# Performance work log

Measured on AMD Instinct MI355X. Metric: run time of the kernel, lower is better.

## Reference

```python
import jax, jax.numpy as jnp
import numpy as np

L, V, P, D, H, F = 6, 50257, 1024, 1024, 16, 4096
DH = D // H
EPS = 1e-5


def setup_inputs() -> dict:
    key = jax.random.key(0)
    ks = jax.random.split(key, 8)
    s = 0.02  # init scale to keep activations sane across layers
    inp = {
        "input_ids": jax.random.randint(ks[0], (2, 1024), 0, V),
        "wte": jax.random.normal(ks[1], (V, D), jnp.float32) * s,
        "wpe": jax.random.normal(ks[2], (P, D), jnp.float32) * s,
        "ln1_g": jnp.ones((L, D), jnp.float32),
        "ln1_b": jnp.zeros((L, D), jnp.float32),
        "wq": jax.random.normal(ks[3], (L, D, D), jnp.float32) * s,
        "bq": jnp.zeros((L, D), jnp.float32),
        "wk": jax.random.normal(ks[4], (L, D, D), jnp.float32) * s,
        "bk": jnp.zeros((L, D), jnp.float32),
        "wv": jax.random.normal(ks[5], (L, D, D), jnp.float32) * s,
        "bv": jnp.zeros((L, D), jnp.float32),
        "wo": jax.random.normal(jax.random.fold_in(key, 10), (L, D, D), jnp.float32) * s,
        "bo": jnp.zeros((L, D), jnp.float32),
        "ln2_g": jnp.ones((L, D), jnp.float32),
        "ln2_b": jnp.zeros((L, D), jnp.float32),
        "w1": jax.random.normal(ks[6], (L, D, F), jnp.float32) * s,
        "b1": jnp.zeros((L, F), jnp.float32),
        "w2": jax.random.normal(ks[7], (L, F, D), jnp.float32) * s,
        "b2": jnp.zeros((L, D), jnp.float32),
        "lnf_g": jnp.ones((D,), jnp.float32),
        "lnf_b": jnp.zeros((D,), jnp.float32),
    }
    return inp


def _ln(x, g, b):
    m = jnp.mean(x, axis=-1, keepdims=True)
    v = jnp.mean(jnp.square(x - m), axis=-1, keepdims=True)
    return (x - m) * jax.lax.rsqrt(v + EPS) * g + b


def _block(x, p):
    (g1, be1, wq, bq, wk, bk, wv, bv, wo, bo, g2, be2, w1, b1, w2, b2) = p
    B, T, _ = x.shape
    h = _ln(x, g1, be1)
    q = (h @ wq + bq).reshape(B, T, H, DH)
    k = (h @ wk + bk).reshape(B, T, H, DH)
    v = (h @ wv + bv).reshape(B, T, H, DH)
    scores = jnp.einsum("bqhd,bkhd->bhqk", q, k) * (1.0 / np.sqrt(DH))
    attn = jax.nn.softmax(scores, axis=-1)  # NOTE: no causal mask (as in source)
    o = jnp.einsum("bhqk,bkhd->bqhd", attn, v).reshape(B, T, D)
    x = x + o @ wo + bo
    h2 = _ln(x, g2, be2)
    x = x + jax.nn.gelu(h2 @ w1 + b1, approximate=False) @ w2 + b2
    return x


def reference(input_ids, wte, wpe, ln1_g, ln1_b, wq, bq, wk, bk, wv, bv,
              wo, bo, ln2_g, ln2_b, w1, b1, w2, b2, lnf_g, lnf_b):
    T = input_ids.shape[1]
    x = wte[input_ids] + wpe[:T]  # [B,T,D]
    params = (ln1_g, ln1_b, wq, bq, wk, bk, wv, bv, wo, bo,
              ln2_g, ln2_b, w1, b1, w2, b2)

    def step(x, p):
        return _block(x, p), None

    x, _ = jax.lax.scan(step, x, params)
    return _ln(x, lnf_g, lnf_b)
```

## Files before the change

### kernel.cpp

```cpp
#include <hip/hip_runtime.h>
#include <hip/hip_bf16.h>
#include <math.h>

#define DV 1024
#define FF 4096
#define NLAY 6
#define NH 16
#define TT 1024
#define NTOK 2048

typedef float f32x4 __attribute__((ext_vector_type(4)));
typedef short bf16x8 __attribute__((ext_vector_type(8)));
typedef unsigned short u16;
typedef u16 u16x4 __attribute__((ext_vector_type(4)));
typedef u16 u16x8 __attribute__((ext_vector_type(8)));

__device__ __forceinline__ u16 f2b(float f) {
  unsigned u = __float_as_uint(f);
  unsigned r = (u + 0x7fffu + ((u >> 16) & 1u)) >> 16;
  return (u16)r;
}
__device__ __forceinline__ float b2f(u16 u) {
  return __uint_as_float(((unsigned)u) << 16);
}

__device__ __forceinline__ void gload_lds16(const void* g, void* lds) {
  __builtin_amdgcn_global_load_lds(
      (const __attribute__((address_space(1))) void*)g,
      (__attribute__((address_space(3))) void*)lds, 16, 0, 0);
}

__global__ __launch_bounds__(256) void embed_ln_k(const int* __restrict__ ids,
                                                  const float* __restrict__ wte,
                                                  const float* __restrict__ wpe,
                                                  const float* __restrict__ gg,
                                                  const float* __restrict__ bb,
                                                  float* __restrict__ X,
                                                  u16* __restrict__ outb) {
  int row = blockIdx.x, tid = threadIdx.x;
  int t = row & (TT - 1);
  int id = ids[row];
  f32x4 a = *(const f32x4*)(wte + (size_t)id * DV + tid * 4);
  f32x4 p = *(const f32x4*)(wpe + (size_t)t * DV + tid * 4);
  f32x4 v = a + p;
  *(f32x4*)(X + (size_t)row * DV + tid * 4) = v;
  float s1 = v[0] + v[1] + v[2] + v[3];
  float s2 = v[0] * v[0] + v[1] * v[1] + v[2] * v[2] + v[3] * v[3];
#pragma unroll
  for (int o = 32; o >= 1; o >>= 1) {
    s1 += __shfl_xor(s1, o);
    s2 += __shfl_xor(s2, o);
  }
  __shared__ float sh[8];
  int w = tid >> 6;
  if ((tid & 63) == 0) { sh[w] = s1; sh[w + 4] = s2; }
  __syncthreads();
  s1 = sh[0] + sh[1] + sh[2] + sh[3];
  s2 = sh[4] + sh[5] + sh[6] + sh[7];
  float mean = s1 * (1.0f / DV);
  float var = s2 * (1.0f / DV) - mean * mean;
  float rstd = rsqrtf(var + 1e-5f);
  f32x4 gv = *(const f32x4*)(gg + tid * 4);
  f32x4 bv = *(const f32x4*)(bb + tid * 4);
  u16x4 r;
#pragma unroll
  for (int i = 0; i < 4; ++i) r[i] = f2b((v[i] - mean) * rstd * gv[i] + bv[i]);
  *(u16x4*)(outb + (size_t)row * DV + tid * 4) = r;
}

template <int OUTF>
__global__ __launch_bounds__(256) void ln_k(const float* __restrict__ X,
                                            const float* __restrict__ gg,
                                            const float* __restrict__ bb,
                                            u16* __restrict__ outb,
                                            float* __restrict__ outf) {
  int row = blockIdx.x, tid = threadIdx.x;
  f32x4 v = *(const f32x4*)(X + (size_t)row * DV + tid * 4);
  float s1 = v[0] + v[1] + v[2] + v[3];
  float s2 = v[0] * v[0] + v[1] * v[1] + v[2] * v[2] + v[3] * v[3];
#pragma unroll
  for (int o = 32; o >= 1; o >>= 1) {
    s1 += __shfl_xor(s1, o);
    s2 += __shfl_xor(s2, o);
  }
  __shared__ float sh[8];
  int w = tid >> 6;
  if ((tid & 63) == 0) { sh[w] = s1; sh[w + 4] = s2; }
  __syncthreads();
  s1 = sh[0] + sh[1] + sh[2] + sh[3];
  s2 = sh[4] + sh[5] + sh[6] + sh[7];
  float mean = s1 * (1.0f / DV);
  float var = s2 * (1.0f / DV) - mean * mean;
  float rstd = rsqrtf(var + 1e-5f);
  f32x4 gv = *(const f32x4*)(gg + tid * 4);
  f32x4 bv = *(const f32x4*)(bb + tid * 4);
  f32x4 o;
#pragma unroll
  for (int i = 0; i < 4; ++i) o[i] = (v[i] - mean) * rstd * gv[i] + bv[i];
  if (OUTF) {
    *(f32x4*)(outf + (size_t)row * DV + tid * 4) = o;
  } else {
    u16x4 r = {f2b(o[0]), f2b(o[1]), f2b(o[2]), f2b(o[3])};
    *(u16x4*)(outb + (size_t)row * DV + tid * 4) = r;
  }
}

template <int NS, int OUTF>
__global__ __launch_bounds__(256) void reduce_ln_k(
    float* __restrict__ X, const u16* __restrict__ pp,
    const float* __restrict__ bias, const float* __restrict__ gg,
    const float* __restrict__ bb, u16* __restrict__ outb,
    float* __restrict__ outf) {
  int row = blockIdx.x, tid = threadIdx.x;
  size_t off = (size_t)row * DV + tid * 4;
  f32x4 v = *(const f32x4*)(X + off);
  if (NS > 0) {
    f32x4 bvv = *(const f32x4*)(bias + tid * 4);
    v += bvv;
#pragma unroll
    for (int s = 0; s < NS; ++s) {
      u16x4 pv = *(const u16x4*)(pp + (size_t)s * NTOK * DV + off);
      v[0] += b2f(pv[0]); v[1] += b2f(pv[1]);
      v[2] += b2f(pv[2]); v[3] += b2f(pv[3]);
    }
    *(f32x4*)(X + off) = v;
  }
  float s1 = v[0] + v[1] + v[2] + v[3];
  float s2 = v[0] * v[0] + v[1] * v[1] + v[2] * v[2] + v[3] * v[3];
#pragma unroll
  for (int o = 32; o >= 1; o >>= 1) {
    s1 += __shfl_xor(s1, o);
    s2 += __shfl_xor(s2, o);
  }
  __shared__ float sh[8];
  int w = tid >> 6;
  if ((tid & 63) == 0) { sh[w] = s1; sh[w + 4] = s2; }
  __syncthreads();
  s1 = sh[0] + sh[1] + sh[2] + sh[3];
  s2 = sh[4] + sh[5] + sh[6] + sh[7];
  float mean = s1 * (1.0f / DV);
  float var = s2 * (1.0f / DV) - mean * mean;
  float rstd = rsqrtf(var + 1e-5f);
  f32x4 gv = *(const f32x4*)(gg + tid * 4);
  f32x4 bv = *(const f32x4*)(bb + tid * 4);
  f32x4 o;
#pragma unroll
  for (int i = 0; i < 4; ++i) o[i] = (v[i] - mean) * rstd * gv[i] + bv[i];
  if (OUTF) {
    *(f32x4*)(outf + off) = o;
  } else {
    u16x4 r = {f2b(o[0]), f2b(o[1]), f2b(o[2]), f2b(o[3])};
    *(u16x4*)(outb + off) = r;
  }
}

__global__ __launch_bounds__(256) void transw_k(const float* __restrict__ wq,
                                                const float* __restrict__ wk,
                                                const float* __restrict__ wv,
                                                const float* __restrict__ wo,
                                                const float* __restrict__ w1,
                                                const float* __restrict__ w2,
                                                u16* __restrict__ WT) {
  int lay = blockIdx.y;
  size_t oDD = (size_t)lay * DV * DV, oDF = (size_t)lay * DV * FF;
  u16* WTL = WT + (size_t)lay * 12 * 1024 * 1024;
  int bid = blockIdx.x;
  const float* src;
  u16* dst;
  int K, N, tile;
  if (bid < 256) {
    int which = bid >> 6;
    src = (which == 0 ? wq : which == 1 ? wk : which == 2 ? wv : wo) + oDD;
    dst = WTL + (size_t)which * (DV * DV);
    K = DV; N = DV; tile = bid & 63;
  } else if (bid < 512) {
    src = w1 + oDF; dst = WTL + (size_t)4 * (DV * DV); K = DV; N = FF; tile = bid - 256;
  } else {
    src = w2 + oDF; dst = WTL + (size_t)8 * (DV * DV); K = FF; N = DV; tile = bid - 512;
  }
  int ntc = N >> 8;
  int tr = tile / ntc, tc = tile - tr * ntc;
  int k0 = tr * 64, n0 = tc * 256;
  __shared__ u16 ts[64][258];
  int tid = threadIdx.x, l = tid & 63, w = tid >> 6;
  f32x4 vv[16];
#pragma unroll
  for (int i = 0; i < 16; ++i)
    vv[i] = *(const f32x4*)(src + (size_t)(k0 + i * 4 + w) * N + n0 + l * 4);
#pragma unroll
  for (int i = 0; i < 16; ++i) {
    u16x4 c = {f2b(vv[i][0]), f2b(vv[i][1]), f2b(vv[i][2]), f2b(vv[i][3])};
    *(u16x4*)(&ts[i * 4 + w][l * 4]) = c;
  }
  __syncthreads();
  int kk = (tid & 7) * 8, nn = tid >> 3;
#pragma unroll
  for (int j = 0; j < 8; ++j) {
    int n = j * 32 + nn;
    u16x8 ov;
#pragma unroll
    for (int m = 0; m < 8; ++m) ov[m] = ts[kk + m][n];
    *(u16x8*)(dst + (size_t)(n0 + n) * K + k0 + kk) = ov;
  }
}

template <int EPI>
__global__ __launch_bounds__(512) void gemm_k(
    const u16* __restrict__ A, const u16* __restrict__ Wt,
    const float* __restrict__ b0, const float* __restrict__ b1,
    const float* __restrict__ b2v, u16* __restrict__ o0, u16* __restrict__ o1,
    u16* __restrict__ o2t, u16* __restrict__ op, float* __restrict__ of,
    const float* __restrict__ res, int M, int N, int K, int KS) {
  int z = blockIdx.z;
  const u16* W = Wt;
  const float* bias = b0;
  u16* outb = o0;
  if (EPI == 0) {
    W = Wt + (size_t)z * N * K;
    bias = z == 0 ? b0 : z == 1 ? b1 : b2v;
    outb = z == 0 ? o0 : o1;
  }
  int gx = gridDim.x, nwg = gx * gridDim.y;
  int lin = blockIdx.y * gx + blockIdx.x;
  int cpx = nwg >> 3;
  int swz = (lin & 7) * cpx + (lin >> 3);
  int bm = (swz % gx) * 128, bn = (swz / gx) * 128;
  int kbeg = (EPI == 3) ? z * KS : 0;
  int klen = (EPI == 3) ? KS : K;
  __shared__ __attribute__((aligned(16))) u16 SM[32768];
  u16* As = SM;
  u16* Bs = SM + 16384;
  u16* Cs = SM;
  int tid = threadIdx.x, l = tid & 63, w = tid >> 6;
  int q = l & 15, g = l >> 4;
  int wm = (w >> 1) * 32, wn = (w & 1) * 64;
  int srow = w * 16 + (l >> 3);
  int scol = (((l & 7) ^ ((l >> 3) & 7))) * 8;
  const u16* Ab = A + (size_t)(bm + srow) * K + kbeg + scol;
  const u16* Wb = W + (size_t)(bn + srow) * K + kbeg + scol;
  f32x4 acc[2][4] = {};
  int nk = klen >> 6;
#pragma unroll
  for (int i = 0; i < 2; ++i) {
    gload_lds16(Ab + (size_t)i * 8 * K, &As[(w * 16 + i * 8) * 64]);
    gload_lds16(Wb + (size_t)i * 8 * K, &Bs[(w * 16 + i * 8) * 64]);
  }
  __syncthreads();
  for (int t = 0; t < nk; ++t) {
    int cur = t & 1;
    if (t + 1 < nk) {
      int ko = (t + 1) * 64;
#pragma unroll
      for (int i = 0; i < 2; ++i) {
        gload_lds16(Ab + (size_t)i * 8 * K + ko,
                    &As[(cur ^ 1) * 8192 + (w * 16 + i * 8) * 64]);
        gload_lds16(Wb + (size_t)i * 8 * K + ko,
                    &Bs[(cur ^ 1) * 8192 + (w * 16 + i * 8) * 64]);
      }
    }
#pragma unroll
    for (int kk = 0; kk < 2; ++kk) {
      bf16x8 af[2], bfr[4];
#pragma unroll
      for (int f = 0; f < 2; ++f) {
        int ra = wm + f * 16 + q;
        af[f] = *(const bf16x8*)(&As[cur * 8192 + ra * 64 + ((kk * 4 + g) ^ (ra & 7)) * 8]);
      }
#pragma unroll
      for (int f = 0; f < 4; ++f) {
        int rb = wn + f * 16 + q;
        bfr[f] = *(const bf16x8*)(&Bs[cur * 8192 + rb * 64 + ((kk * 4 + g) ^ (rb & 7)) * 8]);
      }
#pragma unroll
      for (int fm = 0; fm < 2; ++fm)
#pragma unroll
        for (int fn = 0; fn < 4; ++fn)
          acc[fm][fn] = __builtin_amdgcn_mfma_f32_16x16x32_bf16(af[fm], bfr[fn],
                                                                acc[fm][fn], 0, 0, 0);
    }
    __syncthreads();
  }
  if (EPI == 2) {
#pragma unroll
    for (int fm = 0; fm < 2; ++fm)
#pragma unroll
      for (int fn = 0; fn < 4; ++fn) {
        int gcol = bn + wn + fn * 16 + q;
        int growb = bm + wm + fm * 16 + g * 4;
        float bv = bias[gcol];
#pragma unroll
        for (int r = 0; r < 4; ++r)
          of[(size_t)(growb + r) * N + gcol] = res[(size_t)(growb + r) * N + gcol]
                                               + acc[fm][fn][r] + bv;
      }
    return;
  }
  bool tr = (EPI == 0 && z == 2);
#pragma unroll
  for (int fm = 0; fm < 2; ++fm) {
#pragma unroll
    for (int fn = 0; fn < 4; ++fn) {
      int cL = wn + fn * 16 + q;
      float bv = (EPI == 3) ? 0.0f : bias[bn + cL];
#pragma unroll
      for (int r = 0; r < 4; ++r) {
        int rL = wm + fm * 16 + g * 4 + r;
        float v = acc[fm][fn][r] + bv;
        if (EPI == 1) v = 0.5f * v * (1.0f + erff(v * 0.70710678118f));
        if (EPI == 0 && z == 0) v *= 0.125f;
        if (tr) Cs[cL * 132 + rL] = f2b(v);
        else    Cs[rL * 132 + cL] = f2b(v);
      }
    }
  }
  __syncthreads();
  {
    int rowL = tid >> 4, c8 = (tid & 15) * 8;
#pragma unroll
    for (int p = 0; p < 4; ++p) {
      int row = p * 32 + rowL;
      u16x4 lo = *(const u16x4*)(&Cs[row * 132 + c8]);
      u16x4 hi = *(const u16x4*)(&Cs[row * 132 + c8 + 4]);
      u16x8 ov = {lo[0], lo[1], lo[2], lo[3], hi[0], hi[1], hi[2], hi[3]};
      if (tr) {
        *(u16x8*)(o2t + (size_t)(bn + row) * M + bm + c8) = ov;
      } else if (EPI == 3) {
        *(u16x8*)(op + (size_t)z * M * N + (size_t)(bm + row) * N + bn + c8) = ov;
      } else {
        *(u16x8*)(outb + (size_t)(bm + row) * N + bn + c8) = ov;
      }
    }
  }
}

__global__ __launch_bounds__(256) void attn_k(const u16* __restrict__ Q,
                                              const u16* __restrict__ Kb,
                                              const u16* __restrict__ Vt,
                                              u16* __restrict__ O) {
  int bid = blockIdx.x;
  int qt = bid & 15, h = (bid >> 4) & 15, b = bid >> 8;
  int tid = threadIdx.x, l = tid & 63, w = tid >> 6;
  int q = l & 15, g = l >> 4;
  int tokbase = b * TT;
  int qbase = tokbase + qt * 64 + w * 16;
  __shared__ __attribute__((aligned(16))) u16 Ks[2][64 * 64];
  __shared__ __attribute__((aligned(16))) u16 Vs[2][64 * 64];
  __shared__ __attribute__((aligned(16))) u16 Ps[4][1024];
  bf16x8 qf[2];
  {
    int qrow = qbase + q;
#pragma unroll
    for (int half = 0; half < 2; ++half)
      qf[half] = *(const bf16x8*)(Q + (size_t)qrow * DV + h * 64 + half * 32 + g * 8);
  }
  int rr = tid >> 3, cc = tid & 7;
  const u16* ksrc = Kb + (size_t)(tokbase + rr) * DV + h * 64 + ((cc ^ (rr & 7)) * 8);
  const u16* vsrc = Vt + (size_t)(h * 64 + rr) * NTOK + tokbase + ((cc ^ (rr & 7)) * 8);
  const size_t kst = (size_t)32 * DV;
  const size_t vst = (size_t)32 * NTOK;
  f32x4 oacc[4] = {};
  float m_run = -INFINITY, l_run = 0.0f;
#define AST(bb_, t)                                                      \
  {                                                                      \
    gload_lds16(ksrc + (size_t)(t) * 64 * DV, &Ks[bb_][tid * 8]);        \
    gload_lds16(ksrc + (size_t)(t) * 64 * DV + kst, &Ks[bb_][2048 + tid * 8]); \
    gload_lds16(vsrc + (t) * 64, &Vs[bb_][tid * 8]);                     \
    gload_lds16(vsrc + (t) * 64 + vst, &Vs[bb_][2048 + tid * 8]);        \
  }
  AST(0, 0);
  __syncthreads();
  const int nkb = TT / 64;
  for (int kbk = 0; kbk < nkb; ++kbk) {
    int cur = kbk & 1;
    if (kbk + 1 < nkb) AST(cur ^ 1, kbk + 1);
    f32x4 s[4] = {};
#pragma unroll
    for (int kt = 0; kt < 4; ++kt) {
      int row = kt * 16 + q;
#pragma unroll
      for (int half = 0; half < 2; ++half) {
        int chunk = (half * 4 + g) ^ (row & 7);
        bf16x8 kf = *(const bf16x8*)(&Ks[cur][row * 64 + chunk * 8]);
        s[kt] = __builtin_amdgcn_mfma_f32_16x16x32_bf16(kf, qf[half], s[kt], 0, 0, 0);
      }
    }
    float tmax = -INFINITY;
#pragma unroll
    for (int kt = 0; kt < 4; ++kt)
#pragma unroll
      for (int r = 0; r < 4; ++r) tmax = fmaxf(tmax, s[kt][r]);
    tmax = fmaxf(tmax, __shfl_xor(tmax, 16));
    tmax = fmaxf(tmax, __shfl_xor(tmax, 32));
    if (!__all(tmax <= m_run + 8.0f)) {
      float m_new = fmaxf(m_run, tmax);
      float corr = __expf(m_run - m_new);
      float corr4[4];
#pragma unroll
      for (int r = 0; r < 4; ++r) corr4[r] = __shfl(corr, g * 4 + r);
#pragma unroll
      for (int nt = 0; nt < 4; ++nt)
#pragma unroll
        for (int r = 0; r < 4; ++r) oacc[nt][r] *= corr4[r];
      l_run *= corr;
      m_run = m_new;
    }
    float psum = 0.0f;
    u16x4 pb[4];
#pragma unroll
    for (int kt = 0; kt < 4; ++kt)
#pragma unroll
      for (int r = 0; r < 4; ++r) {
        float p = __expf(s[kt][r] - m_run);
        psum += p;
        pb[kt][r] = f2b(p);
      }
    psum += __shfl_xor(psum, 16);
    psum += __shfl_xor(psum, 32);
    l_run += psum;
#pragma unroll
    for (int kt = 0; kt < 4; ++kt)
      *(u16x4*)(&Ps[w][q * 64 + ((kt * 4 + g) ^ (q & 7)) * 4]) = pb[kt];
#pragma unroll
    for (int kt2 = 0; kt2 < 2; ++kt2) {
      int c0 = kt2 * 8 + (g >> 1) * 4 + (g & 1) * 2;
      u16x4 a0 = *(const u16x4*)(&Ps[w][q * 64 + ((c0) ^ (q & 7)) * 4]);
      u16x4 a1 = *(const u16x4*)(&Ps[w][q * 64 + ((c0 + 1) ^ (q & 7)) * 4]);
      bf16x8 pa = {(short)a0[0], (short)a0[1], (short)a0[2], (short)a0[3],
                   (short)a1[0], (short)a1[1], (short)a1[2], (short)a1[3]};
#pragma unroll
      for (int nt = 0; nt < 4; ++nt) {
        int vrow = nt * 16 + q;
        int vc = (kt2 * 4 + g) ^ (vrow & 7);
        bf16x8 vf = *(const bf16x8*)(&Vs[cur][vrow * 64 + vc * 8]);
        oacc[nt] = __builtin_amdgcn_mfma_f32_16x16x32_bf16(pa, vf, oacc[nt], 0, 0, 0);
      }
    }
    __syncthreads();
  }
#undef AST
  float rl[4];
#pragma unroll
  for (int r = 0; r < 4; ++r) rl[r] = 1.0f / __shfl(l_run, g * 4 + r);
#pragma unroll
  for (int nt = 0; nt < 4; ++nt)
#pragma unroll
    for (int r = 0; r < 4; ++r) {
      int qrw = qbase + g * 4 + r;
      int d = nt * 16 + q;
      O[(size_t)qrw * DV + h * 64 + d] = f2b(oacc[nt][r] * rl[r]);
    }
}

extern "C" void kernel_launch(void* const* d_in, const int* in_sizes, int n_in,
                              void* d_out, int out_size, void* d_ws, size_t ws_size,
                              hipStream_t stream) {
  const int*   ids = (const int*)d_in[0];
  const float* wte = (const float*)d_in[1];
  const float* wpe = (const float*)d_in[2];
  const float* l1g = (const float*)d_in[3];
  const float* l1b = (const float*)d_in[4];
  const float* wq  = (const float*)d_in[5];
  const float* bq  = (const float*)d_in[6];
  const float* wk  = (const float*)d_in[7];
  const float* bk  = (const float*)d_in[8];
  const float* wv  = (const float*)d_in[9];
  const float* bv  = (const float*)d_in[10];
  const float* wo  = (const float*)d_in[11];
  const float* bo  = (const float*)d_in[12];
  const float* l2g = (const float*)d_in[13];
  const float* l2b = (const float*)d_in[14];
  const float* w1  = (const float*)d_in[15];
  const float* b1  = (const float*)d_in[16];
  const float* w2  = (const float*)d_in[17];
  const float* b2  = (const float*)d_in[18];
  const float* lfg = (const float*)d_in[19];
  const float* lfb = (const float*)d_in[20];
  (void)in_sizes; (void)n_in; (void)out_size;

  bool bigws = ws_size >= ((size_t)221 << 20);
  bool midws = ws_size >= ((size_t)101 << 20);

  char* ws = (char*)d_ws;
  float* x   = (float*)(ws + 0);
  u16*   hb  = (u16*)(ws + ((size_t)8 << 20));
  u16*   qb  = (u16*)(ws + ((size_t)12 << 20));
  u16*   kb  = (u16*)(ws + ((size_t)16 << 20));
  u16*   vbt = (u16*)(ws + ((size_t)20 << 20));
  u16*   ab  = (u16*)(ws + ((size_t)24 << 20));
  u16*   mb  = (u16*)(ws + ((size_t)28 << 20));
  u16*   pp  = (u16*)(ws + ((size_t)44 << 20));
  u16*   WT  = (u16*)(ws + ((size_t)(midws ? 76 : 44) << 20));

  if (bigws)
    transw_k<<<dim3(768, 6), 256, 0, stream>>>(wq, wk, wv, wo, w1, w2, WT);
  embed_ln_k<<<NTOK, 256, 0, stream>>>(ids, wte, wpe, l1g, l1b, x, hb);

  for (int lay = 0; lay < NLAY; ++lay) {
    size_t oDD = (size_t)lay * DV * DV;
    size_t oDF = (size_t)lay * DV * FF;
    u16* WTL = bigws ? WT + (size_t)lay * 12 * 1024 * 1024 : WT;
    if (!bigws)
      transw_k<<<dim3(768, 1), 256, 0, stream>>>(wq + oDD, wk + oDD, wv + oDD,
                                                 wo + oDD, w1 + oDF, w2 + oDF, WTL);
    gemm_k<0><<<dim3(16, 8, 3), 512, 0, stream>>>(
        hb, WTL, bq + lay * DV, bk + lay * DV, bv + lay * DV,
        qb, kb, vbt, nullptr, nullptr, nullptr, NTOK, DV, DV, 0);
    attn_k<<<512, 256, 0, stream>>>(qb, kb, vbt, ab);
    if (midws) {
      gemm_k<3><<<dim3(16, 8, 2), 512, 0, stream>>>(
          ab, WTL + (size_t)3 * DV * DV, nullptr, nullptr, nullptr,
          nullptr, nullptr, nullptr, pp, nullptr, nullptr, NTOK, DV, DV, 512);
      reduce_ln_k<2, 0><<<NTOK, 256, 0, stream>>>(
          x, pp, bo + lay * DV, l2g + lay * DV, l2b + lay * DV, hb, nullptr);
    } else {
      gemm_k<2><<<dim3(16, 8, 1), 512, 0, stream>>>(
          ab, WTL + (size_t)3 * DV * DV, bo + lay * DV, nullptr, nullptr,
          nullptr, nullptr, nullptr, nullptr, x, x, NTOK, DV, DV, 0);
      ln_k<0><<<NTOK, 256, 0, stream>>>(x, l2g + lay * DV, l2b + lay * DV, hb, nullptr);
    }
    gemm_k<1><<<dim3(16, 32, 1), 512, 0, stream>>>(
        hb, WTL + (size_t)4 * DV * DV, b1 + lay * FF, nullptr, nullptr,
        mb, nullptr, nullptr, nullptr, nullptr, nullptr, NTOK, FF, DV, 0);
    if (midws) {
      gemm_k<3><<<dim3(16, 8, 4), 512, 0, stream>>>(
          mb, WTL + (size_t)8 * DV * DV, nullptr, nullptr, nullptr,
          nullptr, nullptr, nullptr, pp, nullptr, nullptr, NTOK, DV, FF, 1024);
      if (lay < NLAY - 1)
        reduce_ln_k<4, 0><<<NTOK, 256, 0, stream>>>(
            x, pp, b2 + lay * DV, l1g + (lay + 1) * DV, l1b + (lay + 1) * DV,
            hb, nullptr);
      else
        reduce_ln_k<4, 1><<<NTOK, 256, 0, stream>>>(
            x, pp, b2 + lay * DV, lfg, lfb, nullptr, (float*)d_out);
    } else {
      gemm_k<2><<<dim3(16, 8, 1), 512, 0, stream>>>(
          mb, WTL + (size_t)8 * DV * DV, b2 + lay * DV, nullptr, nullptr,
          nullptr, nullptr, nullptr, nullptr, x, x, NTOK, DV, FF, 0);
      if (lay < NLAY - 1)
        ln_k<0><<<NTOK, 256, 0, stream>>>(x, l1g + (lay + 1) * DV,
                                          l1b + (lay + 1) * DV, hb, nullptr);
      else
        ln_k<1><<<NTOK, 256, 0, stream>>>(x, lfg, lfb, nullptr, (float*)d_out);
    }
  }
}
```

Before: 870.6 us.

## Add 256x128-tile GEMM kernel for FFN up and down projections

Adds a new gemm256_k kernel with 256x128 output tiles, 8 waves each computing a 64x64 subtile (4x4 MFMA fragments), double-buffered LDS staging and a workgroup swizzle. The FFN up-projection (with GELU epilogue) and the split-K down-projection now use it instead of the 128x128 gemm_k. The larger tile raises arithmetic intensity and cuts global loads per FLOP. In exchange it uses more registers and LDS per block, which may lower occupancy, and it launches fewer workgroups (256 for the up-projection and for the split-K down-projection). The GELU line is removed from gemm_k, which is now dead code for EPI 1.

```diff
diff --git a/kernel.cpp b/kernel.cpp
--- a/kernel.cpp
+++ b/kernel.cpp
@@ -306,7 +306,6 @@
       for (int r = 0; r < 4; ++r) {
         int rL = wm + fm * 16 + g * 4 + r;
         float v = acc[fm][fn][r] + bv;
-        if (EPI == 1) v = 0.5f * v * (1.0f + erff(v * 0.70710678118f));
         if (EPI == 0 && z == 0) v *= 0.125f;
         if (tr) Cs[cL * 132 + rL] = f2b(v);
         else    Cs[rL * 132 + cL] = f2b(v);
@@ -328,6 +327,100 @@
         *(u16x8*)(op + (size_t)z * M * N + (size_t)(bm + row) * N + bn + c8) = ov;
       } else {
         *(u16x8*)(outb + (size_t)(bm + row) * N + bn + c8) = ov;
+      }
+    }
+  }
+}
+
+template <int EPI>
+__global__ __launch_bounds__(512) void gemm256_k(
+    const u16* __restrict__ A, const u16* __restrict__ Wt,
+    const float* __restrict__ b0, u16* __restrict__ o0, u16* __restrict__ op,
+    int M, int N, int K, int KS) {
+  int z = blockIdx.z;
+  int gx = gridDim.x, nwg = gx * gridDim.y;
+  int lin = blockIdx.y * gx + blockIdx.x;
+  int cpx = nwg >> 3;
+  int swz = (lin & 7) * cpx + (lin >> 3);
+  int bm = (swz % gx) * 256, bn = (swz / gx) * 128;
+  int kbeg = (EPI == 3) ? z * KS : 0;
+  int klen = (EPI == 3) ? KS : K;
+  __shared__ __attribute__((aligned(16))) u16 SM[49152];
+  u16* As = SM;
+  u16* Bs = SM + 32768;
+  u16* Cs = SM;
+  int tid = threadIdx.x, l = tid & 63, w = tid >> 6;
+  int q = l & 15, g = l >> 4;
+  int wm = (w >> 1) * 64, wn = (w & 1) * 64;
+  int srowA = w * 32 + (l >> 3);
+  int srowB = w * 16 + (l >> 3);
+  int scol = (((l & 7) ^ ((l >> 3) & 7))) * 8;
+  const u16* Ab = A + (size_t)(bm + srowA) * K + kbeg + scol;
+  const u16* Wb = Wt + (size_t)(bn + srowB) * K + kbeg + scol;
+  f32x4 acc[4][4] = {};
+  int nk = klen >> 6;
+#define STG256(buf, ko)                                                       \
+  {                                                                           \
+    _Pragma("unroll") for (int i = 0; i < 4; ++i)                             \
+        gload_lds16(Ab + (size_t)(i * 8) * K + (ko),                          \
+                    &As[(buf) * 16384 + (w * 32 + i * 8) * 64]);              \
+    _Pragma("unroll") for (int i = 0; i < 2; ++i)                             \
+        gload_lds16(Wb + (size_t)(i * 8) * K + (ko),                          \
+                    &Bs[(buf) * 8192 + (w * 16 + i * 8) * 64]);               \
+  }
+  STG256(0, 0);
+  __syncthreads();
+  for (int t = 0; t < nk; ++t) {
+    int cur = t & 1;
+    if (t + 1 < nk) STG256(cur ^ 1, (t + 1) * 64);
+#pragma unroll
+    for (int kk = 0; kk < 2; ++kk) {
+      bf16x8 af[4], bfr[4];
+#pragma unroll
+      for (int f = 0; f < 4; ++f) {
+        int ra = wm + f * 16 + q;
+        af[f] = *(const bf16x8*)(&As[cur * 16384 + ra * 64 + ((kk * 4 + g) ^ (ra & 7)) * 8]);
+        int rb = wn + f * 16 + q;
+        bfr[f] = *(const bf16x8*)(&Bs[cur * 8192 + rb * 64 + ((kk * 4 + g) ^ (rb & 7)) * 8]);
+      }
+#pragma unroll
+      for (int fm = 0; fm < 4; ++fm)
+#pragma unroll
+        for (int fn = 0; fn < 4; ++fn)
+          acc[fm][fn] = __builtin_amdgcn_mfma_f32_16x16x32_bf16(af[fm], bfr[fn],
+                                                                acc[fm][fn], 0, 0, 0);
+    }
+    __syncthreads();
+  }
+#undef STG256
+#pragma unroll
+  for (int fm = 0; fm < 4; ++fm) {
+#pragma unroll
+    for (int fn = 0; fn < 4; ++fn) {
+      int cL = wn + fn * 16 + q;
+      float bv = (EPI == 3) ? 0.0f : b0[bn + cL];
+#pragma unroll
+      for (int r = 0; r < 4; ++r) {
+        int rL = wm + fm * 16 + g * 4 + r;
+        float v = acc[fm][fn][r] + bv;
+        if (EPI == 1) v = 0.5f * v * (1.0f + erff(v * 0.70710678118f));
+        Cs[rL * 132 + cL] = f2b(v);
+      }
+    }
+  }
+  __syncthreads();
+  {
+    int rowL = tid >> 4, c8 = (tid & 15) * 8;
+#pragma unroll
+    for (int p = 0; p < 8; ++p) {
+      int row = p * 32 + rowL;
+      u16x4 lo = *(const u16x4*)(&Cs[row * 132 + c8]);
+      u16x4 hi = *(const u16x4*)(&Cs[row * 132 + c8 + 4]);
+      u16x8 ov = {lo[0], lo[1], lo[2], lo[3], hi[0], hi[1], hi[2], hi[3]};
+      if (EPI == 3) {
+        *(u16x8*)(op + (size_t)z * M * N + (size_t)(bm + row) * N + bn + c8) = ov;
+      } else {
+        *(u16x8*)(o0 + (size_t)(bm + row) * N + bn + c8) = ov;
       }
     }
   }
@@ -518,13 +611,13 @@
           nullptr, nullptr, nullptr, nullptr, x, x, NTOK, DV, DV, 0);
       ln_k<0><<<NTOK, 256, 0, stream>>>(x, l2g + lay * DV, l2b + lay * DV, hb, nullptr);
     }
-    gemm_k<1><<<dim3(16, 32, 1), 512, 0, stream>>>(
-        hb, WTL + (size_t)4 * DV * DV, b1 + lay * FF, nullptr, nullptr,
-        mb, nullptr, nullptr, nullptr, nullptr, nullptr, NTOK, FF, DV, 0);
+    gemm256_k<1><<<dim3(8, 32), 512, 0, stream>>>(
+        hb, WTL + (size_t)4 * DV * DV, b1 + lay * FF, mb, nullptr,
+        NTOK, FF, DV, 0);
     if (midws) {
-      gemm_k<3><<<dim3(16, 8, 4), 512, 0, stream>>>(
-          mb, WTL + (size_t)8 * DV * DV, nullptr, nullptr, nullptr,
-          nullptr, nullptr, nullptr, pp, nullptr, nullptr, NTOK, DV, FF, 1024);
+      gemm256_k<3><<<dim3(8, 8, 4), 512, 0, stream>>>(
+          mb, WTL + (size_t)8 * DV * DV, nullptr, nullptr, pp,
+          NTOK, DV, FF, 1024);
       if (lay < NLAY - 1)
         reduce_ln_k<4, 0><<<NTOK, 256, 0, stream>>>(
             x, pp, b2 + lay * DV, l1g + (lay + 1) * DV, l1b + (lay + 1) * DV,
```

New measurement: 901.5 us. 1.04x slower.
